# Optimization experiments

Measured on AMD Instinct MI355X. Metric: run time of the kernel, lower is better.

## Reference

```python
import jax, jax.numpy as jnp
import numpy as np

B, N, D, K, H, S = 4, 4096, 768, 8, 128, 64
EPS = 1e-5


def _ln(x, g, b):
    m = jnp.mean(x, axis=-1, keepdims=True)
    v = jnp.var(x, axis=-1, keepdims=True)
    return (x - m) / jnp.sqrt(v + EPS) * g + b


def setup_inputs() -> dict:
    key = jax.random.key(0)
    ks = jax.random.split(key, 20)
    coordinates = jax.random.uniform(ks[0], (B, N, 3)) * 5.0  # room-scale coords
    features = jax.random.normal(ks[1], (B, N, D))
    superpoint_labels = jax.random.randint(ks[2], (B, N), 0, S).astype(jnp.int32)
    s = 0.02
    # geometric_encoder: Linear(4,H//2) LN ReLU Linear(H//2,D) LN
    Hg = H // 2
    W1 = jax.random.normal(ks[3], (4, Hg)) * s
    b1 = jnp.zeros((Hg,))
    g1 = jnp.ones((Hg,)); bt1 = jnp.zeros((Hg,))
    W2 = jax.random.normal(ks[4], (Hg, D)) * s
    b2 = jnp.zeros((D,))
    g2 = jnp.ones((D,)); bt2 = jnp.zeros((D,))
    # superpoint_aggregator: Linear(D,H) LN ReLU Linear(H,D) LN
    A1 = jax.random.normal(ks[5], (D, H)) * s
    ab1 = jnp.zeros((H,))
    ag1 = jnp.ones((H,)); abt1 = jnp.zeros((H,))
    A2 = jax.random.normal(ks[6], (H, D)) * s
    ab2 = jnp.zeros((D,))
    ag2 = jnp.ones((D,)); abt2 = jnp.zeros((D,))
    return dict(coordinates=coordinates, features=features,
                superpoint_labels=superpoint_labels,
                W1=W1, b1=b1, g1=g1, bt1=bt1, W2=W2, b2=b2, g2=g2, bt2=bt2,
                A1=A1, ab1=ab1, ag1=ag1, abt1=abt1, A2=A2, ab2=ab2, ag2=ag2, abt2=abt2)


def _forward(coordinates, features, superpoint_labels,
             W1, b1, g1, bt1, W2, b2, g2, bt2,
             A1, ab1, ag1, abt1, A2, ab2, ag2, abt2):
    # ---- KNN (squared distances give same ordering as cdist) ----
    d2 = jnp.sum((coordinates[:, :, None, :] - coordinates[:, None, :, :]) ** 2, axis=-1)  # [B,N,N]
    _, idx = jax.lax.top_k(-d2, K + 1)            # ascending distance
    knn = idx[:, :, 1:]                            # drop self, [B,N,K]
    nbr = jax.vmap(lambda c, i: c[i])(coordinates, knn)          # [B,N,K,3]
    rel = nbr - coordinates[:, :, None, :]                       # [B,N,K,3]
    rd = jnp.linalg.norm(rel, axis=-1, keepdims=True)            # [B,N,K,1]
    geom = jnp.concatenate([rd, rel[..., 0:1], rel[..., 1:2], jnp.minimum(rd, 1.0)], axis=-1)  # [B,N,K,4]
    h = jax.nn.relu(_ln(geom @ W1 + b1, g1, bt1))
    enc = _ln(h @ W2 + b2, g2, bt2)                              # [B,N,K,D]
    geometric_context = jnp.mean(enc, axis=2)                    # [B,N,D]
    # ---- superpoint masked-reduce / scatter-update ----
    seg = (superpoint_labels + jnp.arange(B, dtype=superpoint_labels.dtype)[:, None] * S).reshape(-1)
    sums = jax.ops.segment_sum(features.reshape(B * N, D), seg, num_segments=B * S).reshape(B, S, D)
    cnt = jax.ops.segment_sum(jnp.ones((B * N,), features.dtype), seg, num_segments=B * S).reshape(B, S)
    means = sums / jnp.maximum(cnt, 1.0)[..., None]              # [B,S,D]
    ah = jax.nn.relu(_ln(means @ A1 + ab1, ag1, abt1))
    agg = _ln(ah @ A2 + ab2, ag2, abt2)                          # [B,S,D]
    agg_p = jax.vmap(lambda a, l: a[l])(agg, superpoint_labels)  # [B,N,D]
    cnt_p = jax.vmap(lambda c, l: c[l])(cnt, superpoint_labels)  # [B,N]
    w = 0.1
    upd = (1.0 - w) * features + w * agg_p
    enhanced = jnp.where((cnt_p >= 2.0)[..., None], upd, features)
    return enhanced + 0.1 * geometric_context


def reference(coordinates, features, superpoint_labels,
              W1, b1, g1, bt1, W2, b2, g2, bt2,
              A1, ab1, ag1, abt1, A2, ab2, ag2, abt2):
    return _forward(coordinates, features, superpoint_labels,
                    W1, b1, g1, bt1, W2, b2, g2, bt2,
                    A1, ab1, ag1, abt1, A2, ab2, ag2, abt2)
```

## Files before the change

kernel.cpp:

```cpp
#include <hip/hip_runtime.h>
#include <math.h>

typedef short v8s __attribute__((ext_vector_type(8)));
typedef short v4sh __attribute__((ext_vector_type(4)));
typedef float v4f __attribute__((ext_vector_type(4)));

#define EPS 1e-5f

__device__ __forceinline__ unsigned short f2bf(float x){
  unsigned u = __float_as_uint(x);
  return (unsigned short)((u + 0x7fffu + ((u>>16)&1u)) >> 16);
}
__device__ __forceinline__ float bf2f(unsigned short us){
  return __uint_as_float(((unsigned)us)<<16);
}

__global__ __launch_bounds__(256) void k_prep(const float* __restrict__ W2,
                                              const float* __restrict__ b2,
                                              unsigned short* __restrict__ Gm,
                                              float* __restrict__ w2bar,
                                              float* __restrict__ ubar,
                                              float* __restrict__ scal,
                                              unsigned short* __restrict__ W2T,
                                              const float* __restrict__ A1,
                                              const float* __restrict__ A2,
                                              unsigned short* __restrict__ A1bf,
                                              unsigned short* __restrict__ A2bf)
{
  __shared__ float row[768];
  __shared__ float part[256];
  int t = threadIdx.x;
  int blk = blockIdx.x;
  if (blk < 64){
    for (int c = t; c < 768; c += 256) row[c] = W2[blk*768 + c];
    __syncthreads();
    int jp = t & 63, quarter = t >> 6;
    float acc = 0.f;
    int c0 = quarter*192;
    for (int c = c0; c < c0+192; ++c) acc += row[c]*W2[jp*768 + c];
    part[t] = acc;
    __syncthreads();
    if (t < 64){
      float sv = part[t] + part[t+64] + part[t+128] + part[t+192];
      Gm[blk*64 + t] = f2bf(sv * (1.f/768.f));
    }
  } else if (blk == 64){
    if (t < 64){
      float sw=0.f, sus=0.f;
      for (int c=0;c<768;++c){ float wv=W2[t*768+c]; sw+=wv; sus+=wv*b2[c]; }
      w2bar[t]=sw*(1.f/768.f); ubar[t]=sus*(1.f/768.f);
    } else if (t == 64){
      float sb=0.f, sb2=0.f;
      for (int c=0;c<768;++c){ float v=b2[c]; sb+=v; sb2+=v*v; }
      scal[0]=sb*(1.f/768.f); scal[1]=sb2*(1.f/768.f);
    }
  } else if (blk < 113){
    int bi = blk - 65;
    int c0 = bi*16;
    for (int idx = t; idx < 1024; idx += 256){
      int c = c0 + (idx >> 6), j = idx & 63;
      W2T[c*64 + j] = f2bf(W2[j*768 + c]);
    }
  } else if (blk < 209){
    int base = (blk-113)*1024 + t*4;
    v4f v = *reinterpret_cast<const v4f*>(&A1[base]);
    v4sh p;
    #pragma unroll
    for (int e=0;e<4;++e) p[e] = (short)f2bf(v[e]);
    *reinterpret_cast<v4sh*>(&A1bf[base]) = p;
  } else {
    int base = (blk-209)*1024 + t*4;
    v4f v = *reinterpret_cast<const v4f*>(&A2[base]);
    v4sh p;
    #pragma unroll
    for (int e=0;e<4;++e) p[e] = (short)f2bf(v[e]);
    *reinterpret_cast<v4sh*>(&A2bf[base]) = p;
  }
}

__global__ __launch_bounds__(256) void k_sortidx(const int* __restrict__ labels,
                                                 unsigned short* __restrict__ idxbuf,
                                                 int* __restrict__ offs,
                                                 float* __restrict__ cntw)
{
  __shared__ int hist[64];
  __shared__ int base[64];
  __shared__ int lab[4096];
  int t = threadIdx.x;
  int b = blockIdx.x;
  if (t < 64) hist[t] = 0;
  __syncthreads();
  for (int i=t;i<4096;i+=256){
    int l = labels[b*4096 + i];
    lab[i] = l;
    atomicAdd(&hist[l], 1);
  }
  __syncthreads();
  if (t < 64){
    int v = hist[t];
    int x = v;
    #pragma unroll
    for (int d=1; d<64; d<<=1){
      int y = __shfl_up(x, d, 64);
      if (t >= d) x += y;
    }
    base[t] = x - v;
    offs[b*64 + t] = x - v;
    cntw[b*64 + t] = (float)v;
  }
  __syncthreads();
  for (int i=t;i<4096;i+=256){
    int pos = atomicAdd(&base[lab[i]], 1);
    idxbuf[b*4096 + pos] = (unsigned short)i;
  }
}

__global__ __launch_bounds__(256) void k_segsum2(const float* __restrict__ features,
                                                 const unsigned short* __restrict__ idxbuf,
                                                 const int* __restrict__ offs,
                                                 const float* __restrict__ cntw,
                                                 float* __restrict__ mean)
{
  __shared__ unsigned short ridx[4096];
  int t = threadIdx.x;
  int blk = blockIdx.x;
  int b = blk / 192;
  int rem = blk - b*192;
  int seg = rem / 3, cc = rem - seg*3;
  int off = offs[b*64 + seg];
  int n = (int)cntw[b*64 + seg];
  for (int i=t;i<n;i+=256) ridx[i] = idxbuf[b*4096 + off + i];
  __syncthreads();
  int col = cc*256 + t;
  const float* fb = features + (size_t)b*4096*768 + col;
  float acc = 0.f;
  int i = 0;
  for (; i+8<=n; i+=8){
    float v0 = fb[(size_t)ridx[i+0]*768];
    float v1 = fb[(size_t)ridx[i+1]*768];
    float v2 = fb[(size_t)ridx[i+2]*768];
    float v3 = fb[(size_t)ridx[i+3]*768];
    float v4 = fb[(size_t)ridx[i+4]*768];
    float v5 = fb[(size_t)ridx[i+5]*768];
    float v6 = fb[(size_t)ridx[i+6]*768];
    float v7 = fb[(size_t)ridx[i+7]*768];
    acc += v0+v1+v2+v3+v4+v5+v6+v7;
  }
  for (; i<n; ++i) acc += fb[(size_t)ridx[i]*768];
  mean[((size_t)(b*64 + seg))*768 + col] = acc / fmaxf((float)n, 1.f);
}

__global__ __launch_bounds__(1024) void k_knn(const float* __restrict__ coords,
                                              float* __restrict__ geom)
{
#pragma clang fp contract(off)
  __shared__ __align__(16) char pool[147968];
  float2*             cxy   = (float2*)pool;
  float*              czp   = (float*)(pool + 32768);
  unsigned*           listD = (unsigned*)(pool + 49152);
  unsigned short*     listI = (unsigned short*)(pool + 114688);
  unsigned long long* spill = (unsigned long long*)(pool + 49152);
  unsigned*           thr   = (unsigned*)(pool + 147456);
  unsigned*           cnt   = (unsigned*)(pool + 147712);

  int t = threadIdx.x;
  int b  = blockIdx.x >> 6;
  int qb = blockIdx.x & 63;
  const float* cb = coords + (size_t)b*4096*3;
  for (int n = t; n < 4096; n += 1024){
    float x = cb[n*3+0], y = cb[n*3+1], z = cb[n*3+2];
    cxy[n] = make_float2(x, y); czp[n] = z;
  }
  if (t < 64) cnt[t] = 0;
  __syncthreads();

  int q = t & 63, c = t >> 6;
  int nq = qb*64 + q;
  float2 qxy = cxy[nq]; float qz = czp[nq];
  int j0 = c*256;

  unsigned long long kv[9];
  #pragma unroll
  for (int i=0;i<9;++i) kv[i] = ~0ull;
  for (int jj=0; jj<32; ++jj){
    int j = j0 + jj;
    float2 pxy = cxy[j]; float pz = czp[j];
    float dx = pxy.x - qxy.x, dy = pxy.y - qxy.y, dz = pz - qz;
    float d2 = dx*dx; d2 = d2 + dy*dy; d2 = d2 + dz*dz;
    unsigned long long key = ((unsigned long long)__float_as_uint(d2) << 32) | (unsigned)j;
    if (key < kv[8]){
      kv[8] = key;
      #pragma unroll
      for (int i=8;i>0;--i){
        bool sw = kv[i] < kv[i-1];
        unsigned long long lo = sw ? kv[i] : kv[i-1];
        unsigned long long hi = sw ? kv[i-1] : kv[i];
        kv[i-1] = lo; kv[i] = hi;
      }
    }
  }
  {
    unsigned long long* srow = spill + ((q*16 + c)*10);
    #pragma unroll
    for (int i=0;i<9;++i) srow[i] = kv[i];
    srow[9] = ~0ull;
  }
  __syncthreads();

  {
    int mq = t >> 4, mc = t & 15;
    unsigned long long* srow = spill + ((mq*16 + mc)*10);
    int pc = 0;
    unsigned long long head = srow[0];
    unsigned long long m = 0;
    for (int r=0; r<9; ++r){
      m = head;
      #pragma unroll
      for (int s=1; s<16; s<<=1){
        unsigned long long o = __shfl_xor(m, s, 16);
        m = (o < m) ? o : m;
      }
      if (head == m){ pc++; head = srow[pc]; }
    }
    if (mc == 0) thr[mq] = (unsigned)(m >> 32);
  }
  __syncthreads();

  unsigned thrq = thr[q];
  for (int jj=0; jj<256; ++jj){
    int j = j0 + jj;
    float2 pxy = cxy[j]; float pz = czp[j];
    float dx = pxy.x - qxy.x, dy = pxy.y - qxy.y, dz = pz - qz;
    float d2 = dx*dx; d2 = d2 + dy*dy; d2 = d2 + dz*dz;
    unsigned db = __float_as_uint(d2);
    if (db <= thrq){
      unsigned pos = atomicAdd(&cnt[q], 1u);
      if (pos < 256u){
        listD[q*256 + pos] = db;
        listI[q*256 + pos] = (unsigned short)j;
      }
    }
  }
  __syncthreads();

  int mq = t >> 4, mc = t & 15;
  unsigned craw = cnt[mq];
  unsigned cq = craw > 256u ? 256u : craw;
  unsigned long long key[16];
  #pragma unroll
  for (int i=0;i<16;++i){
    int slot = mc + i*16;
    if ((unsigned)slot < cq)
      key[i] = (((unsigned long long)listD[mq*256 + slot]) << 32) | listI[mq*256 + slot];
    else
      key[i] = ~0ull;
  }
  int mnq = qb*64 + mq;
  float2 mqxy = cxy[mnq];
  float* outp = geom + ((size_t)(b*4096 + mnq))*32;
  unsigned long long mprev = 0;
  for (int pick=0; pick<9; ++pick){
    unsigned long long lmin = ~0ull;
    #pragma unroll
    for (int i=0;i<16;++i){
      unsigned long long kk = key[i];
      bool ok = (pick == 0) | (kk > mprev);
      lmin = (ok && kk < lmin) ? kk : lmin;
    }
    unsigned long long m = lmin;
    #pragma unroll
    for (int s=1; s<16; s<<=1){
      unsigned long long o = __shfl_xor(m, s, 16);
      m = (o < m) ? o : m;
    }
    if (pick > 0 && mc == 0){
      unsigned bi = (unsigned)(m & 0xFFFFFFFFu);
      float d2w = __uint_as_float((unsigned)(m >> 32));
      float2 nb = cxy[bi];
      float rx = nb.x - mqxy.x, ry = nb.y - mqxy.y;
      float rd = sqrtf(d2w);
      v4f g; g[0]=rd; g[1]=rx; g[2]=ry; g[3]=fminf(rd,1.0f);
      *reinterpret_cast<v4f*>(outp + (pick-1)*4) = g;
    }
    mprev = m;
  }

  bool fb = (craw > 256u);
  if (__any(fb)){
    if (fb){
      unsigned long long kv2[9];
      #pragma unroll
      for (int i=0;i<9;++i) kv2[i] = ~0ull;
      int jj0 = mc*256;
      for (int jj=0; jj<256; ++jj){
        int j = jj0 + jj;
        float2 pxy = cxy[j]; float pz = czp[j];
        float dx = pxy.x - mqxy.x, dy = pxy.y - mqxy.y, dz = pz - czp[mnq];
        float d2 = dx*dx; d2 = d2 + dy*dy; d2 = d2 + dz*dz;
        unsigned long long kkey = ((unsigned long long)__float_as_uint(d2) << 32) | (unsigned)j;
        if (kkey < kv2[8]){
          kv2[8] = kkey;
          #pragma unroll
          for (int i=8;i>0;--i){
            bool sw = kv2[i] < kv2[i-1];
            unsigned long long lo = sw ? kv2[i] : kv2[i-1];
            unsigned long long hi = sw ? kv2[i-1] : kv2[i];
            kv2[i-1] = lo; kv2[i] = hi;
          }
        }
      }
      int pc = 0;
      for (int pick=0; pick<9; ++pick){
        unsigned long long head = ~0ull;
        #pragma unroll
        for (int i=0;i<9;++i) head = (pc == i) ? kv2[i] : head;
        unsigned long long m = head;
        #pragma unroll
        for (int s=1; s<16; s<<=1){
          unsigned long long o = __shfl_xor(m, s, 16);
          m = (o < m) ? o : m;
        }
        if (head == m) pc++;
        if (pick > 0 && mc == 0){
          unsigned bi = (unsigned)(m & 0xFFFFFFFFu);
          float d2w = __uint_as_float((unsigned)(m >> 32));
          float2 nb = cxy[bi];
          float rx = nb.x - mqxy.x, ry = nb.y - mqxy.y;
          float rd = sqrtf(d2w);
          v4f g; g[0]=rd; g[1]=rx; g[2]=ry; g[3]=fminf(rd,1.0f);
          *reinterpret_cast<v4f*>(outp + (pick-1)*4) = g;
        }
      }
    }
  }
}

__global__ __launch_bounds__(256) void k_hbuild(
    const float* __restrict__ geom,
    const float* __restrict__ W1, const float* __restrict__ b1,
    const float* __restrict__ g1, const float* __restrict__ bt1,
    const unsigned short* __restrict__ Gm,
    const float* __restrict__ w2bar, const float* __restrict__ ubar,
    const float* __restrict__ scal,
    unsigned short* __restrict__ hprime, float* __restrict__ S1, float* __restrict__ S2)
{
  __shared__ v8s htile_v[256*8];
  __shared__ __align__(16) float sW1[256];
  __shared__ __align__(16) float sb1[64], sg1[64], sbt1[64], swb[64], su[64];
  __shared__ float sinv[256], sminv[256];
  int t = threadIdx.x;
  sW1[t] = W1[t];
  if (t < 64){ sb1[t]=b1[t]; sg1[t]=g1[t]; sbt1[t]=bt1[t]; swb[t]=w2bar[t]; su[t]=ubar[t]; }
  int r0 = blockIdx.x * 256;
  v4f gv = reinterpret_cast<const v4f*>(geom)[r0 + t];
  __syncthreads();
  float t1[64];
  #pragma unroll
  for (int l=0;l<64;l+=4){
    v4f w0 = *reinterpret_cast<const v4f*>(&sW1[l]);
    v4f w1 = *reinterpret_cast<const v4f*>(&sW1[64+l]);
    v4f w2 = *reinterpret_cast<const v4f*>(&sW1[128+l]);
    v4f w3 = *reinterpret_cast<const v4f*>(&sW1[192+l]);
    v4f bb = *reinterpret_cast<const v4f*>(&sb1[l]);
    #pragma unroll
    for (int e=0;e<4;++e)
      t1[l+e] = bb[e] + gv[0]*w0[e] + gv[1]*w1[e] + gv[2]*w2[e] + gv[3]*w3[e];
  }
  float s=0.f, s2=0.f;
  #pragma unroll
  for (int l=0;l<64;++l){ s += t1[l]; s2 += t1[l]*t1[l]; }
  float mu = s*(1.f/64.f);
  float var = s2*(1.f/64.f) - mu*mu;
  float inv = 1.0f/sqrtf(var+EPS);
  #pragma unroll
  for (int l=0;l<64;++l){
    float hv = (t1[l]-mu)*inv*sg1[l] + sbt1[l];
    t1[l] = hv > 0.f ? hv : 0.f;
  }
  #pragma unroll
  for (int cc=0;cc<8;++cc){
    v8s pk;
    #pragma unroll
    for (int e=0;e<8;++e) pk[e] = (short)f2bf(t1[cc*8+e]);
    htile_v[t*8 + (cc ^ (t&7))] = pk;
  }
  __syncthreads();
  int lane = t & 63, w = t >> 6;
  int l15 = lane & 15, l4 = lane >> 4;
  v8s gf[8];
  const v8s* Gv = reinterpret_cast<const v8s*>(Gm);
  #pragma unroll
  for (int tc=0;tc<4;++tc)
    #pragma unroll
    for (int kk=0;kk<2;++kk)
      gf[tc*2+kk] = Gv[(tc*16+l15)*8 + kk*4 + l4];
  float b2bar = scal[0], c0v = scal[1];
  const unsigned short* hs = reinterpret_cast<const unsigned short*>(htile_v);
  for (int rt = w; rt < 16; rt += 4){
    int arow = rt*16 + l15;
    v8s af0 = htile_v[arow*8 + ((l4)   ^ (arow&7))];
    v8s af1 = htile_v[arow*8 + ((4+l4) ^ (arow&7))];
    v4f acc[4];
    #pragma unroll
    for (int tc=0;tc<4;++tc){
      acc[tc] = (v4f){0.f,0.f,0.f,0.f};
      acc[tc] = __builtin_amdgcn_mfma_f32_16x16x32_bf16(af0, gf[tc*2+0], acc[tc], 0,0,0);
      acc[tc] = __builtin_amdgcn_mfma_f32_16x16x32_bf16(af1, gf[tc*2+1], acc[tc], 0,0,0);
    }
    float zh[4]={0,0,0,0}, hwb[4]={0,0,0,0}, hu[4]={0,0,0,0};
    #pragma unroll
    for (int r=0;r<4;++r){
      int row = rt*16 + l4*4 + r;
      #pragma unroll
      for (int tc=0;tc<4;++tc){
        int col = tc*16 + l15;
        int chunk = col >> 3;
        unsigned short us = hs[row*64 + ((chunk ^ (row&7))<<3) + (col&7)];
        float hval = bf2f(us);
        zh[r] += acc[tc][r]*hval;
        hwb[r] += hval*swb[col];
        hu[r]  += hval*su[col];
      }
    }
    #pragma unroll
    for (int mk=1; mk<16; mk<<=1){
      #pragma unroll
      for (int r=0;r<4;++r){
        zh[r] += __shfl_xor(zh[r], mk, 64);
        hwb[r]+= __shfl_xor(hwb[r],mk, 64);
        hu[r] += __shfl_xor(hu[r], mk, 64);
      }
    }
    if (l15 == 0){
      #pragma unroll
      for (int r=0;r<4;++r){
        int row = rt*16 + l4*4 + r;
        float mm = hwb[r] + b2bar;
        float vv = zh[r] + 2.f*hu[r] + c0v - mm*mm;
        float iv = 1.0f/sqrtf(vv + EPS);
        sinv[row]  = iv;
        sminv[row] = mm*iv;
      }
    }
  }
  __syncthreads();
  int p = t >> 3, jg = t & 7;
  float hp[8] = {0,0,0,0,0,0,0,0};
  #pragma unroll
  for (int k=0;k<8;++k){
    int row = p*8 + k;
    float iv = sinv[row];
    v8s hv8 = htile_v[row*8 + (jg ^ (row&7))];
    #pragma unroll
    for (int e=0;e<8;++e) hp[e] += iv * bf2f((unsigned short)hv8[e]);
  }
  v8s pk;
  #pragma unroll
  for (int e=0;e<8;++e) pk[e] = (short)f2bf(hp[e]);
  int gp = blockIdx.x*32 + p;
  reinterpret_cast<v8s*>(hprime)[gp*8 + jg] = pk;
  if (jg == 0){
    float a=0.f, bb=0.f;
    #pragma unroll
    for (int k=0;k<8;++k){ a += sinv[p*8+k]; bb += sminv[p*8+k]; }
    S1[gp]=a; S2[gp]=bb;
  }
}

__global__ __launch_bounds__(256) void k_mlp1(
    const float* __restrict__ mean,
    const unsigned short* __restrict__ A1bf, const float* __restrict__ ab1,
    const float* __restrict__ ag1, const float* __restrict__ abt1,
    unsigned short* __restrict__ ahbuf)
{
  __shared__ float mean4[4][768];
  __shared__ float red[4][4][128];
  __shared__ float t1s[4][128];
  int t = threadIdx.x;
  int row0 = blockIdx.x*4;
  #pragma unroll
  for (int g=0; g<3; ++g){
    int idx = t + g*256;
    int r = idx / 192, q4 = idx - r*192;
    v4f v = *reinterpret_cast<const v4f*>(mean + (size_t)(row0+r)*768 + q4*4);
    mean4[r][q4*4+0]=v[0]; mean4[r][q4*4+1]=v[1];
    mean4[r][q4*4+2]=v[2]; mean4[r][q4*4+3]=v[3];
  }
  __syncthreads();
  int kg = t >> 6, lane = t & 63;
  const unsigned* A1u = (const unsigned*)A1bf;
  float acc0[4] = {0,0,0,0}, acc1[4] = {0,0,0,0};
  int jbeg = kg*192;
  #pragma unroll 8
  for (int j=jbeg; j<jbeg+192; ++j){
    unsigned u = A1u[j*64 + lane];
    float a0 = bf2f((unsigned short)(u & 0xffffu));
    float a1v = bf2f((unsigned short)(u >> 16));
    #pragma unroll
    for (int r=0;r<4;++r){
      float mv = mean4[r][j];
      acc0[r] += mv*a0; acc1[r] += mv*a1v;
    }
  }
  #pragma unroll
  for (int r=0;r<4;++r){
    red[kg][r][lane*2+0] = acc0[r];
    red[kg][r][lane*2+1] = acc1[r];
  }
  __syncthreads();
  #pragma unroll
  for (int o=0; o<2; ++o){
    int idx = t + o*256;
    int r = idx >> 7, c = idx & 127;
    t1s[r][c] = red[0][r][c]+red[1][r][c]+red[2][r][c]+red[3][r][c] + ab1[c];
  }
  __syncthreads();
  int w = t >> 6;
  float x0 = t1s[w][lane], x1 = t1s[w][lane+64];
  float s = x0+x1, s2 = x0*x0+x1*x1;
  #pragma unroll
  for (int mk=1; mk<64; mk<<=1){
    s  += __shfl_xor(s, mk, 64);
    s2 += __shfl_xor(s2, mk, 64);
  }
  float mu = s*(1.f/128.f);
  float var = s2*(1.f/128.f) - mu*mu;
  float iv = 1.0f/sqrtf(var+EPS);
  float a0 = (x0-mu)*iv*ag1[lane]    + abt1[lane];
  float a1v= (x1-mu)*iv*ag1[lane+64] + abt1[lane+64];
  a0 = fmaxf(a0, 0.f); a1v = fmaxf(a1v, 0.f);
  int grow = row0 + w;
  ahbuf[grow*128 + lane]      = f2bf(a0);
  ahbuf[grow*128 + lane + 64] = f2bf(a1v);
}

__global__ __launch_bounds__(256) void k_mlp2(
    const unsigned short* __restrict__ ahbuf,
    const unsigned short* __restrict__ A2bf, const float* __restrict__ ab2,
    const float* __restrict__ ag2, const float* __restrict__ abt2,
    float* __restrict__ agg)
{
  __shared__ float ahl[4][128];
  __shared__ float2 red[4][256];
  __shared__ float2 sst[4];
  int t = threadIdx.x;
  int row0 = blockIdx.x*4;
  #pragma unroll
  for (int o=0;o<2;++o){
    int idx = t + o*256; int r = idx>>7, c = idx&127;
    ahl[r][c] = bf2f(ahbuf[(row0+r)*128 + c]);
  }
  __syncthreads();
  float acc[4][3];
  #pragma unroll
  for (int r=0;r<4;++r){ acc[r][0]=0.f; acc[r][1]=0.f; acc[r][2]=0.f; }
  #pragma unroll 4
  for (int j=0;j<128;++j){
    float f0 = bf2f(A2bf[j*768 + t]);
    float f1 = bf2f(A2bf[j*768 + t + 256]);
    float f2v= bf2f(A2bf[j*768 + t + 512]);
    #pragma unroll
    for (int r=0;r<4;++r){
      float av = ahl[r][j];
      acc[r][0] += av*f0; acc[r][1] += av*f1; acc[r][2] += av*f2v;
    }
  }
  float bb0=ab2[t], bb1=ab2[t+256], bb2=ab2[t+512];
  float o_[4][3];
  #pragma unroll
  for (int r=0;r<4;++r){
    o_[r][0]=acc[r][0]+bb0; o_[r][1]=acc[r][1]+bb1; o_[r][2]=acc[r][2]+bb2;
  }
  #pragma unroll
  for (int r=0;r<4;++r)
    red[r][t] = make_float2(o_[r][0]+o_[r][1]+o_[r][2],
                            o_[r][0]*o_[r][0]+o_[r][1]*o_[r][1]+o_[r][2]*o_[r][2]);
  __syncthreads();
  int w = t>>6, lane = t&63;
  float s=0.f, s2=0.f;
  #pragma unroll
  for (int i=0;i<4;++i){ float2 v = red[w][lane + i*64]; s += v.x; s2 += v.y; }
  #pragma unroll
  for (int mk=1; mk<64; mk<<=1){
    s  += __shfl_xor(s, mk, 64);
    s2 += __shfl_xor(s2, mk, 64);
  }
  if (lane == 0){
    float mu = s*(1.f/768.f);
    float var = s2*(1.f/768.f) - mu*mu;
    sst[w] = make_float2(mu, 1.0f/sqrtf(var+EPS));
  }
  __syncthreads();
  float g0=ag2[t], g1v=ag2[t+256], g2v=ag2[t+512];
  float c0=abt2[t], c1=abt2[t+256], c2=abt2[t+512];
  #pragma unroll
  for (int r=0;r<4;++r){
    float mu = sst[r].x, iv = sst[r].y;
    float* ap = agg + (size_t)(row0+r)*768;
    ap[t]     = (o_[r][0]-mu)*iv*g0 + c0;
    ap[t+256] = (o_[r][1]-mu)*iv*g1v + c1;
    ap[t+512] = (o_[r][2]-mu)*iv*g2v + c2;
  }
}

__global__ __launch_bounds__(256) void k_final(
  const unsigned short* __restrict__ hprime, const unsigned short* __restrict__ W2T,
  const float* __restrict__ S1, const float* __restrict__ S2,
  const float* __restrict__ g2, const float* __restrict__ b2, const float* __restrict__ bt2,
  const float* __restrict__ features, const int* __restrict__ labels,
  const float* __restrict__ cnt, const float* __restrict__ agg,
  float* __restrict__ out)
{
  int t=threadIdx.x; int lane=t&63; int w=t>>6; int l15=lane&15, l4=lane>>4;
  int rowt = blockIdx.x*64 + w*16;
  const v8s* hv = reinterpret_cast<const v8s*>(hprime);
  v8s af0 = hv[(rowt+l15)*8 + l4];
  v8s af1 = hv[(rowt+l15)*8 + 4 + l4];
  float s1r[4], s2r[4], cntr[4]; int labr[4], br[4];
  #pragma unroll
  for (int r=0;r<4;++r){
    int row = rowt + l4*4 + r;
    s1r[r]=S1[row]; s2r[r]=S2[row];
    labr[r]=labels[row]; br[r]=row>>12;
    cntr[r]=cnt[br[r]*64 + labr[r]];
  }
  const v8s* wtv = reinterpret_cast<const v8s*>(W2T);
  for (int tc=0;tc<48;++tc){
    v8s bf0 = wtv[(tc*16+l15)*8 + l4];
    v8s bf1 = wtv[(tc*16+l15)*8 + 4 + l4];
    v4f acc = (v4f){0.f,0.f,0.f,0.f};
    acc = __builtin_amdgcn_mfma_f32_16x16x32_bf16(af0, bf0, acc, 0,0,0);
    acc = __builtin_amdgcn_mfma_f32_16x16x32_bf16(af1, bf1, acc, 0,0,0);
    int c = tc*16 + l15;
    float g2c=g2[c], b2c=b2[c], bt2c=bt2[c];
    #pragma unroll
    for (int r=0;r<4;++r){
      int row = rowt + l4*4 + r;
      float ctxv = 0.1f*(g2c*((acc[r] + b2c*s1r[r] - s2r[r])*0.125f) + bt2c);
      size_t o = (size_t)row*768 + c;
      float f = features[o];
      float av = agg[((size_t)(br[r]*64 + labr[r]))*768 + c];
      float enh = (cntr[r] >= 2.0f) ? (0.9f*f + 0.1f*av) : f;
      out[o] = enh + ctxv;
    }
  }
}

extern "C" void kernel_launch(void* const* d_in, const int* in_sizes, int n_in,
                              void* d_out, int out_size, void* d_ws, size_t ws_size,
                              hipStream_t stream) {
  const float* coords   = (const float*)d_in[0];
  const float* features = (const float*)d_in[1];
  const int*   labels   = (const int*)  d_in[2];
  const float* W1  = (const float*)d_in[3];
  const float* b1  = (const float*)d_in[4];
  const float* g1  = (const float*)d_in[5];
  const float* bt1 = (const float*)d_in[6];
  const float* W2  = (const float*)d_in[7];
  const float* b2  = (const float*)d_in[8];
  const float* g2  = (const float*)d_in[9];
  const float* bt2 = (const float*)d_in[10];
  const float* A1  = (const float*)d_in[11];
  const float* ab1 = (const float*)d_in[12];
  const float* ag1 = (const float*)d_in[13];
  const float* abt1= (const float*)d_in[14];
  const float* A2  = (const float*)d_in[15];
  const float* ab2 = (const float*)d_in[16];
  const float* ag2 = (const float*)d_in[17];
  const float* abt2= (const float*)d_in[18];

  char* ws = (char*)d_ws;
  size_t off = 0;
  auto alloc = [&](size_t bytes){ size_t o = off; off = (off + bytes + 255) & ~(size_t)255; return o; };
  float*          geom   = (float*)(ws + alloc((size_t)131072*4*4));
  unsigned short* hprime = (unsigned short*)(ws + alloc((size_t)16384*64*2));
  float*          S1w    = (float*)(ws + alloc(16384*4));
  float*          S2w    = (float*)(ws + alloc(16384*4));
  unsigned short* W2T    = (unsigned short*)(ws + alloc(768*64*2));
  unsigned short* Gm     = (unsigned short*)(ws + alloc(64*64*2));
  float*          w2bar  = (float*)(ws + alloc(64*4));
  float*          ubar   = (float*)(ws + alloc(64*4));
  float*          scal   = (float*)(ws + alloc(2*4));
  float*          cntw   = (float*)(ws + alloc(4*64*4));
  float*          agg    = (float*)(ws + alloc((size_t)4*64*768*4));
  unsigned short* A1bf   = (unsigned short*)(ws + alloc((size_t)98304*2));
  unsigned short* A2bf   = (unsigned short*)(ws + alloc((size_t)98304*2));
  unsigned short* ahbuf  = (unsigned short*)(ws + alloc((size_t)256*128*2));
  unsigned short* idxbuf = (unsigned short*)(ws + alloc((size_t)4*4096*2));
  int*            offsb  = (int*)(ws + alloc(256*4));
  float*          meanb  = (float*)(ws + alloc((size_t)256*768*4));

  k_prep   <<<dim3(305), dim3(256), 0, stream>>>(W2, b2, Gm, w2bar, ubar, scal, W2T,
                                                 A1, A2, A1bf, A2bf);
  k_sortidx<<<dim3(4),   dim3(256), 0, stream>>>(labels, idxbuf, offsb, cntw);
  k_segsum2<<<dim3(768), dim3(256), 0, stream>>>(features, idxbuf, offsb, cntw, meanb);
  k_mlp1   <<<dim3(64),  dim3(256), 0, stream>>>(meanb, A1bf, ab1, ag1, abt1, ahbuf);
  k_mlp2   <<<dim3(64),  dim3(256), 0, stream>>>(ahbuf, A2bf, ab2, ag2, abt2, agg);
  k_knn    <<<dim3(256), dim3(1024),0, stream>>>(coords, geom);
  k_hbuild <<<dim3(512), dim3(256), 0, stream>>>(geom, W1, b1, g1, bt1, Gm, w2bar, ubar, scal,
                                                 hprime, S1w, S2w);
  k_final  <<<dim3(256), dim3(256), 0, stream>>>(hprime, W2T, S1w, S2w, g2, b2, bt2,
                                                 features, labels, cntw, agg, (float*)d_out);
}
```

Baseline: 280.3 us.

## Restructure KNN kernel to cut LDS footprint and drop spill-based threshold pass

Each query is now handled by a group of 16 contiguous lanes, so the sampled 9th-nearest threshold is found with in-group shuffles instead of a shared-memory spill plus two block barriers. The candidate list stores only 16-bit indices with a smaller cap, and distances are recomputed on load; this shrinks shared memory enough to fit more than one block per CU. Scan start offsets are staggered per lane to reduce LDS bank conflicts, and the sampling heap uses plain floats. The trade-offs are extra distance recomputation and more queries falling back to the full rescan when candidate counts exceed the lower cap.

```diff
diff --git a/kernel.cpp b/kernel.cpp
--- a/kernel.cpp
+++ b/kernel.cpp
@@ -150,19 +150,15 @@
   mean[((size_t)(b*64 + seg))*768 + col] = acc / fmaxf((float)n, 1.f);
 }
 
-__global__ __launch_bounds__(1024) void k_knn(const float* __restrict__ coords,
-                                              float* __restrict__ geom)
+#define KCAP 192
+__global__ __launch_bounds__(1024, 8) void k_knn(const float* __restrict__ coords,
+                                                 float* __restrict__ geom)
 {
 #pragma clang fp contract(off)
-  __shared__ __align__(16) char pool[147968];
-  float2*             cxy   = (float2*)pool;
-  float*              czp   = (float*)(pool + 32768);
-  unsigned*           listD = (unsigned*)(pool + 49152);
-  unsigned short*     listI = (unsigned short*)(pool + 114688);
-  unsigned long long* spill = (unsigned long long*)(pool + 49152);
-  unsigned*           thr   = (unsigned*)(pool + 147456);
-  unsigned*           cnt   = (unsigned*)(pool + 147712);
-
+  __shared__ float2 cxy[4096];
+  __shared__ float  czp[4096];
+  __shared__ unsigned short list[64*KCAP];
+  __shared__ unsigned cnt[64];
   int t = threadIdx.x;
   int b  = blockIdx.x >> 6;
   int qb = blockIdx.x & 63;
@@ -174,128 +170,113 @@
   if (t < 64) cnt[t] = 0;
   __syncthreads();
 
-  int q = t & 63, c = t >> 6;
-  int nq = qb*64 + q;
+  int g = t >> 4, mc = t & 15;
+  int nq = qb*64 + g;
   float2 qxy = cxy[nq]; float qz = czp[nq];
-  int j0 = c*256;
-
-  unsigned long long kv[9];
-  #pragma unroll
-  for (int i=0;i<9;++i) kv[i] = ~0ull;
+  int jb = mc*256;
+
+  float ld[9];
+  #pragma unroll
+  for (int i=0;i<9;++i) ld[i] = __builtin_inff();
   for (int jj=0; jj<32; ++jj){
-    int j = j0 + jj;
+    int x = (jj + 2*mc) & 31;
+    int j = jb + x;
     float2 pxy = cxy[j]; float pz = czp[j];
     float dx = pxy.x - qxy.x, dy = pxy.y - qxy.y, dz = pz - qz;
     float d2 = dx*dx; d2 = d2 + dy*dy; d2 = d2 + dz*dz;
-    unsigned long long key = ((unsigned long long)__float_as_uint(d2) << 32) | (unsigned)j;
-    if (key < kv[8]){
-      kv[8] = key;
+    if (d2 < ld[8]){
+      ld[8] = d2;
       #pragma unroll
       for (int i=8;i>0;--i){
-        bool sw = kv[i] < kv[i-1];
-        unsigned long long lo = sw ? kv[i] : kv[i-1];
-        unsigned long long hi = sw ? kv[i-1] : kv[i];
-        kv[i-1] = lo; kv[i] = hi;
+        bool sw = ld[i] < ld[i-1];
+        float lo = sw ? ld[i] : ld[i-1];
+        float hi = sw ? ld[i-1] : ld[i];
+        ld[i-1] = lo; ld[i] = hi;
       }
     }
   }
-  {
-    unsigned long long* srow = spill + ((q*16 + c)*10);
-    #pragma unroll
-    for (int i=0;i<9;++i) srow[i] = kv[i];
-    srow[9] = ~0ull;
-  }
-  __syncthreads();
-
-  {
-    int mq = t >> 4, mc = t & 15;
-    unsigned long long* srow = spill + ((mq*16 + mc)*10);
-    int pc = 0;
-    unsigned long long head = srow[0];
-    unsigned long long m = 0;
-    for (int r=0; r<9; ++r){
-      m = head;
+  float m = 0.f;
+  for (int r=0; r<9; ++r){
+    m = ld[0];
+    #pragma unroll
+    for (int s=1; s<16; s<<=1){
+      float o = __shfl_xor(m, s, 16);
+      m = fminf(m, o);
+    }
+    if (ld[0] == m){
       #pragma unroll
-      for (int s=1; s<16; s<<=1){
-        unsigned long long o = __shfl_xor(m, s, 16);
-        m = (o < m) ? o : m;
-      }
-      if (head == m){ pc++; head = srow[pc]; }
-    }
-    if (mc == 0) thr[mq] = (unsigned)(m >> 32);
-  }
-  __syncthreads();
-
-  unsigned thrq = thr[q];
+      for (int i=0;i<8;++i) ld[i] = ld[i+1];
+      ld[8] = __builtin_inff();
+    }
+  }
+  unsigned thrq = __float_as_uint(m);
+
   for (int jj=0; jj<256; ++jj){
-    int j = j0 + jj;
+    int x = (jj + 2*mc) & 255;
+    int j = jb + x;
     float2 pxy = cxy[j]; float pz = czp[j];
     float dx = pxy.x - qxy.x, dy = pxy.y - qxy.y, dz = pz - qz;
     float d2 = dx*dx; d2 = d2 + dy*dy; d2 = d2 + dz*dz;
     unsigned db = __float_as_uint(d2);
     if (db <= thrq){
-      unsigned pos = atomicAdd(&cnt[q], 1u);
-      if (pos < 256u){
-        listD[q*256 + pos] = db;
-        listI[q*256 + pos] = (unsigned short)j;
-      }
-    }
-  }
-  __syncthreads();
-
-  int mq = t >> 4, mc = t & 15;
-  unsigned craw = cnt[mq];
-  unsigned cq = craw > 256u ? 256u : craw;
-  unsigned long long key[16];
-  #pragma unroll
-  for (int i=0;i<16;++i){
+      unsigned pos = atomicAdd(&cnt[g], 1u);
+      if (pos < (unsigned)KCAP) list[g*KCAP + pos] = (unsigned short)j;
+    }
+  }
+  __syncthreads();
+
+  unsigned craw = cnt[g];
+  unsigned cq = craw > (unsigned)KCAP ? (unsigned)KCAP : craw;
+  unsigned long long key[12];
+  #pragma unroll
+  for (int i=0;i<12;++i){
     int slot = mc + i*16;
-    if ((unsigned)slot < cq)
-      key[i] = (((unsigned long long)listD[mq*256 + slot]) << 32) | listI[mq*256 + slot];
-    else
-      key[i] = ~0ull;
-  }
-  int mnq = qb*64 + mq;
-  float2 mqxy = cxy[mnq];
-  float* outp = geom + ((size_t)(b*4096 + mnq))*32;
+    if ((unsigned)slot < cq){
+      int j = list[g*KCAP + slot];
+      float2 pxy = cxy[j]; float pz = czp[j];
+      float dx = pxy.x - qxy.x, dy = pxy.y - qxy.y, dz = pz - qz;
+      float d2 = dx*dx; d2 = d2 + dy*dy; d2 = d2 + dz*dz;
+      key[i] = (((unsigned long long)__float_as_uint(d2)) << 32) | (unsigned)j;
+    } else key[i] = ~0ull;
+  }
+  float* outp = geom + ((size_t)(b*4096 + nq))*32;
   unsigned long long mprev = 0;
   for (int pick=0; pick<9; ++pick){
     unsigned long long lmin = ~0ull;
     #pragma unroll
-    for (int i=0;i<16;++i){
+    for (int i=0;i<12;++i){
       unsigned long long kk = key[i];
       bool ok = (pick == 0) | (kk > mprev);
       lmin = (ok && kk < lmin) ? kk : lmin;
     }
-    unsigned long long m = lmin;
+    unsigned long long mm = lmin;
     #pragma unroll
     for (int s=1; s<16; s<<=1){
-      unsigned long long o = __shfl_xor(m, s, 16);
-      m = (o < m) ? o : m;
+      unsigned long long o = __shfl_xor(mm, s, 16);
+      mm = (o < mm) ? o : mm;
     }
     if (pick > 0 && mc == 0){
-      unsigned bi = (unsigned)(m & 0xFFFFFFFFu);
-      float d2w = __uint_as_float((unsigned)(m >> 32));
+      unsigned bi = (unsigned)(mm & 0xFFFFFFFFu);
+      float d2w = __uint_as_float((unsigned)(mm >> 32));
       float2 nb = cxy[bi];
-      float rx = nb.x - mqxy.x, ry = nb.y - mqxy.y;
+      float rx = nb.x - qxy.x, ry = nb.y - qxy.y;
       float rd = sqrtf(d2w);
-      v4f g; g[0]=rd; g[1]=rx; g[2]=ry; g[3]=fminf(rd,1.0f);
-      *reinterpret_cast<v4f*>(outp + (pick-1)*4) = g;
-    }
-    mprev = m;
-  }
-
-  bool fb = (craw > 256u);
+      v4f gg; gg[0]=rd; gg[1]=rx; gg[2]=ry; gg[3]=fminf(rd,1.0f);
+      *reinterpret_cast<v4f*>(outp + (pick-1)*4) = gg;
+    }
+    mprev = mm;
+  }
+
+  bool fb = (craw > (unsigned)KCAP);
   if (__any(fb)){
     if (fb){
       unsigned long long kv2[9];
       #pragma unroll
       for (int i=0;i<9;++i) kv2[i] = ~0ull;
-      int jj0 = mc*256;
       for (int jj=0; jj<256; ++jj){
-        int j = jj0 + jj;
+        int j = jb + jj;
         float2 pxy = cxy[j]; float pz = czp[j];
-        float dx = pxy.x - mqxy.x, dy = pxy.y - mqxy.y, dz = pz - czp[mnq];
+        float dx = pxy.x - qxy.x, dy = pxy.y - qxy.y, dz = pz - qz;
         float d2 = dx*dx; d2 = d2 + dy*dy; d2 = d2 + dz*dz;
         unsigned long long kkey = ((unsigned long long)__float_as_uint(d2) << 32) | (unsigned)j;
         if (kkey < kv2[8]){
@@ -309,26 +290,26 @@
           }
         }
       }
-      int pc = 0;
       for (int pick=0; pick<9; ++pick){
-        unsigned long long head = ~0ull;
-        #pragma unroll
-        for (int i=0;i<9;++i) head = (pc == i) ? kv2[i] : head;
-        unsigned long long m = head;
+        unsigned long long mm = kv2[0];
         #pragma unroll
         for (int s=1; s<16; s<<=1){
-          unsigned long long o = __shfl_xor(m, s, 16);
-          m = (o < m) ? o : m;
+          unsigned long long o = __shfl_xor(mm, s, 16);
+          mm = (o < mm) ? o : mm;
         }
-        if (head == m) pc++;
+        if (kv2[0] == mm){
+          #pragma unroll
+          for (int i=0;i<8;++i) kv2[i] = kv2[i+1];
+          kv2[8] = ~0ull;
+        }
         if (pick > 0 && mc == 0){
-          unsigned bi = (unsigned)(m & 0xFFFFFFFFu);
-          float d2w = __uint_as_float((unsigned)(m >> 32));
+          unsigned bi = (unsigned)(mm & 0xFFFFFFFFu);
+          float d2w = __uint_as_float((unsigned)(mm >> 32));
           float2 nb = cxy[bi];
-          float rx = nb.x - mqxy.x, ry = nb.y - mqxy.y;
+          float rx = nb.x - qxy.x, ry = nb.y - qxy.y;
           float rd = sqrtf(d2w);
-          v4f g; g[0]=rd; g[1]=rx; g[2]=ry; g[3]=fminf(rd,1.0f);
-          *reinterpret_cast<v4f*>(outp + (pick-1)*4) = g;
+          v4f gg; gg[0]=rd; gg[1]=rx; gg[2]=ry; gg[3]=fminf(rd,1.0f);
+          *reinterpret_cast<v4f*>(outp + (pick-1)*4) = gg;
         }
       }
     }
```

Result: slower. 324.1 us (+15.6%).
